# Performance work log

Hardware: AMD Instinct MI355X
Metric: run time of the kernel (lower is better)

Reference implementation:

```python
import jax, jax.numpy as jnp
import numpy as np

B, C, H, W = 4, 64, 256, 256
P, PRIOR, HID, HEADS, NPROMPT = 4, 64, 128, 4, 4
TOKEN = C * P * P  # 1024
RATIO = 0.25


def _patchify(x):
    b, c, h, w = x.shape
    gh, gw = h // P, w // P
    t = x.reshape(b, c, gh, P, gw, P).transpose(0, 2, 4, 1, 3, 5).reshape(b, gh * gw, c * P * P)
    return t, (b, c, gh, gw)


def _unpatchify(t, meta):
    b, c, gh, gw = meta
    return t.reshape(b, gh, gw, c, P, P).transpose(0, 3, 1, 4, 2, 5).reshape(b, c, gh * P, gw * P)


def _coords(gh, gw):
    ys = (jnp.arange(gh, dtype=jnp.float32) + 0.5) / gh
    xs = (jnp.arange(gw, dtype=jnp.float32) + 0.5) / gw
    yy, xx = jnp.meshgrid(ys, xs, indexing='ij')
    return jnp.stack([yy.ravel(), xx.ravel()], axis=-1)  # [N, 2]


def setup_inputs():
    key = jax.random.key(0)
    ks = iter(jax.random.split(key, 32))
    rn = lambda *s: jax.random.normal(next(ks), s, jnp.float32)
    w = lambda *s: rn(*s) * 0.02
    z = lambda *s: jnp.zeros(s, jnp.float32)
    return dict(
        vis_feat=rn(B, C, H, W),
        ir_feat=rn(B, C, H, W),
        prompt_bank=w(NPROMPT, PRIOR),
        Wr=w(2 * C, NPROMPT), br=z(NPROMPT),
        br_Wtok=w(2, 2 * TOKEN, HID), br_Wpri=w(2, PRIOR, HID), br_Wco=w(2, 2, HID),
        br_bs=z(2, HID), br_Wout=w(2, HID), br_bout=z(2),
        br_Wq=w(2, TOKEN, HID), br_Wk=w(2, TOKEN, HID), br_Wv=w(2, TOKEN, HID),
        br_Wo=w(2, HID, TOKEN), br_Wint=w(2, PRIOR, HID),
        br_Wbyp=w(2, 2 * TOKEN, TOKEN), br_bbyp=z(2, TOKEN),
        conv1_w=w(C, C, 3, 3), conv1_b=z(C),
        conv2_w=w(C, C, 3, 3), conv2_b=z(C),
        Wa1=w(PRIOR, 2 * C), ba1=z(2 * C),
        Wa2=w(2 * C, 2 * C), ba2=z(2 * C),
    )


def reference(vis_feat, ir_feat, prompt_bank, Wr, br, br_Wtok, br_Wpri, br_Wco, br_bs, br_Wout, br_bout, br_Wq, br_Wk, br_Wv, br_Wo, br_Wint, br_Wbyp, br_bbyp, conv1_w, conv1_b, conv2_w, conv2_b, Wa1, ba1, Wa2, ba2):
    # intent router: pooled features -> prompt mixture -> intent vector
    pooled = jnp.concatenate([vis_feat.mean((2, 3)), ir_feat.mean((2, 3))], -1)  # [B, 2C]
    prompt_weight = jax.nn.softmax(pooled @ Wr + br, -1)  # [B, NPROMPT]
    intent = prompt_weight @ prompt_bank  # [B, PRIOR]

    def split(x):
        F = jnp.fft.fft2(x)
        return jnp.abs(F), jnp.angle(F)

    vamp, vph = split(vis_feat)
    iamp, iph = split(ir_feat)

    def fuse(vm, im, i):
        vt, meta = _patchify(vm)
        it_, _ = _patchify(im)
        b, c, gh, gw = meta
        n = gh * gw
        coords = _coords(gh, gw)
        # token score net: tokens + intent + coord embedding -> scalar score per token
        h = (jnp.concatenate([vt, it_], -1) @ br_Wtok[i]
             + (intent @ br_Wpri[i])[:, None, :]
             + (coords @ br_Wco[i])[None] + br_bs[i])
        score = jax.nn.gelu(h) @ br_Wout[i] + br_bout[i]  # [B, N]
        k = max(1, int(n * RATIO))
        topk_val, topk_idx = jax.lax.top_k(score, k)
        gth = lambda t: jnp.take_along_axis(t, topk_idx[:, :, None], axis=1)
        vs, irs = gth(vt), gth(it_)  # [B, k, TOKEN]
        # selected-token cross attention (vis queries, ir keys/values), intent-modulated
        dh = HID // HEADS
        hd = lambda x, Wm: (x @ Wm).reshape(b, k, HEADS, dh)
        q, kk, vv = hd(vs, br_Wq[i]), hd(irs, br_Wk[i]), hd(irs, br_Wv[i])
        attn = jax.nn.softmax(jnp.einsum('bqhd,bkhd->bhqk', q, kk) / jnp.float32(np.sqrt(dh)), -1)
        o = jnp.einsum('bhqk,bkhd->bqhd', attn, vv).reshape(b, k, HID)
        o = o + (intent @ br_Wint[i])[:, None, :]
        fused_sel = vs + o @ br_Wo[i]  # [B, k, TOKEN]
        # lightweight bypass on all tokens (gated blend), then scatter selected back
        g = jax.nn.sigmoid(jnp.concatenate([vt, it_], -1) @ br_Wbyp[i] + br_bbyp[i])
        full = g * vt + (1.0 - g) * it_
        full = full.at[jnp.arange(b)[:, None], topk_idx].set(fused_sel)
        return _unpatchify(full, meta)

    famp = fuse(vamp, iamp, 0)
    fph = fuse(vph, iph, 1)
    fph = jnp.arctan2(jnp.sin(fph), jnp.cos(fph))  # phase wrap to (-pi, pi]
    spec = jax.lax.complex(famp * jnp.cos(fph), famp * jnp.sin(fph))
    spatial = jnp.fft.ifft2(spec).real

    conv = lambda x, wgt, bia: jax.lax.conv_general_dilated(
        x, wgt, (1, 1), 'SAME', dimension_numbers=('NCHW', 'OIHW', 'NCHW')) + bia[None, :, None, None]
    y = conv(jax.nn.relu(conv(spatial, conv1_w, conv1_b)), conv2_w, conv2_b)
    aff = jax.nn.gelu(intent @ Wa1 + ba1) @ Wa2 + ba2  # [B, 2C]
    gamma, beta = aff[:, :C], aff[:, C:]
    y = y * (1.0 + 0.1 * jnp.tanh(gamma))[:, :, None, None] + 0.1 * beta[:, :, None, None]
    return y + 0.5 * (vis_feat + ir_feat)
```

## Files before the change

kernel.cpp:

```cpp
#include <hip/hip_runtime.h>

typedef unsigned int uint;
typedef unsigned short ushort;
typedef unsigned long long u64;
typedef __attribute__((ext_vector_type(8))) short short8;
typedef __attribute__((ext_vector_type(4))) float f32x4;

__device__ __forceinline__ uint brev8(uint x){ return __brev(x) >> 24; }
__device__ __forceinline__ float geluf(float x){
  return 0.5f*x*(1.f + tanhf(0.7978845608028654f*(x + 0.044715f*x*x*x)));
}
__device__ __forceinline__ ushort f2bf(float f){
  unsigned u = __float_as_uint(f);
  unsigned r = u + 0x7FFFu + ((u >> 16) & 1u);
  return (ushort)(r >> 16);
}
__device__ __forceinline__ float bf2f(ushort u){
  return __uint_as_float((uint)u << 16);
}

__global__ __launch_bounds__(256) void kern_pool(const float* __restrict__ vis,
                                                 const float* __restrict__ irf,
                                                 float* __restrict__ pooled){
  __shared__ float red[256];
  int bc = blockIdx.x;
  int b = bc >> 7, cc = bc & 127;
  const float* src = (cc < 64) ? (vis + (size_t)(b*64+cc)*65536)
                               : (irf + (size_t)(b*64+(cc-64))*65536);
  float s = 0.f;
  for (int i = threadIdx.x; i < 65536; i += 256) s += src[i];
  red[threadIdx.x] = s;
  __syncthreads();
  for (int off = 128; off > 0; off >>= 1){
    if (threadIdx.x < off) red[threadIdx.x] += red[threadIdx.x + off];
    __syncthreads();
  }
  if (threadIdx.x == 0) pooled[bc] = red[0] * (1.f/65536.f);
}

__global__ __launch_bounds__(256) void kern_small(const float* __restrict__ pooled,
    const float* __restrict__ Wr, const float* __restrict__ br,
    const float* __restrict__ bank, const float* __restrict__ Wpri,
    const float* __restrict__ Wint, const float* __restrict__ Wa1,
    const float* __restrict__ ba1, const float* __restrict__ Wa2,
    const float* __restrict__ ba2,
    float* __restrict__ IP, float* __restrict__ IPint,
    float* __restrict__ modg, float* __restrict__ modb){
  __shared__ float logit_s[16];
  __shared__ float pw_s[16];
  __shared__ float intent_s[4][64];
  __shared__ float t1_s[4][128];
  int t = threadIdx.x;
  if (t < 16){
    int b = t >> 2, j = t & 3;
    float s = br[j];
    for (int k = 0; k < 128; ++k) s += pooled[b*128+k]*Wr[k*4+j];
    logit_s[t] = s;
  }
  __syncthreads();
  if (t < 4){
    int b = t;
    float m = logit_s[b*4];
    for (int j = 1; j < 4; ++j) m = fmaxf(m, logit_s[b*4+j]);
    float e[4], sum = 0.f;
    for (int j = 0; j < 4; ++j){ e[j] = expf(logit_s[b*4+j]-m); sum += e[j]; }
    for (int j = 0; j < 4; ++j) pw_s[b*4+j] = e[j]/sum;
  }
  __syncthreads();
  {
    int b = t >> 6, p = t & 63;
    float s = 0.f;
    for (int j = 0; j < 4; ++j) s += pw_s[b*4+j]*bank[j*64+p];
    intent_s[b][p] = s;
  }
  __syncthreads();
  for (int o = t; o < 1024; o += 256){
    int i = o >> 9, rem = o & 511, b = rem >> 7, n = rem & 127;
    float s1 = 0.f, s2 = 0.f;
    for (int p = 0; p < 64; ++p){
      float iv = intent_s[b][p];
      s1 += iv * Wpri[(i*64+p)*128 + n];
      s2 += iv * Wint[(i*64+p)*128 + n];
    }
    IP[o] = s1; IPint[o] = s2;
  }
  for (int o = t; o < 512; o += 256){
    int b = o >> 7, n = o & 127;
    float s = ba1[n];
    for (int p = 0; p < 64; ++p) s += intent_s[b][p]*Wa1[p*128+n];
    t1_s[b][n] = geluf(s);
  }
  __syncthreads();
  for (int o = t; o < 512; o += 256){
    int b = o >> 7, n = o & 127;
    float s = ba2[n];
    for (int p = 0; p < 128; ++p) s += t1_s[b][p]*Wa2[p*128+n];
    if (n < 64) modg[b*64+n] = 1.f + 0.1f*tanhf(s);
    else        modb[b*64+(n-64)] = 0.1f*s;
  }
}

__global__ __launch_bounds__(256) void kern_fft_rows_fwd(const float* __restrict__ x,
    float* __restrict__ sre, float* __restrict__ sim){
  __shared__ float re[2][256], im[2][256];
  __shared__ float twr[128], twi[128];
  int t = threadIdx.x;
  if (t < 128){
    float a = -6.2831853071795864f * (float)t * (1.f/256.f);
    sincosf(a, &twi[t], &twr[t]);
  }
  int r = t >> 7, jj = t & 127;
  size_t row = (size_t)blockIdx.x*2 + r;
  {
    const float* xp = x + row*256;
    re[r][jj] = xp[jj]; re[r][jj+128] = xp[jj+128];
    im[r][jj] = 0.f;    im[r][jj+128] = 0.f;
  }
  __syncthreads();
  for (int s = 0; s < 8; ++s){
    int half = 128 >> s;
    int j = jj & (half-1);
    int g = jj >> (7-s);
    int k = (g << (8-s)) + j;
    int m = j << s;
    float wc = twr[m], ws = twi[m];
    float are = re[r][k],      aim = im[r][k];
    float bre = re[r][k+half], bim = im[r][k+half];
    re[r][k] = are + bre; im[r][k] = aim + bim;
    float tr = are - bre, ti = aim - bim;
    re[r][k+half] = tr*wc - ti*ws;
    im[r][k+half] = tr*ws + ti*wc;
    __syncthreads();
  }
  {
    float* orp = sre + row*256; float* oip = sim + row*256;
    int w1 = jj, w2 = jj + 128;
    orp[w1] = re[r][brev8(w1)]; oip[w1] = im[r][brev8(w1)];
    orp[w2] = re[r][brev8(w2)]; oip[w2] = im[r][brev8(w2)];
  }
}

__global__ __launch_bounds__(256) void kern_ifft_rows_spec(const float* __restrict__ famp,
    const float* __restrict__ fph, float* __restrict__ sre, float* __restrict__ sim){
  __shared__ float re[4][256], im[4][256];
  __shared__ float twr[128], twi[128];
  int t = threadIdx.x;
  if (t < 128){
    float a = -6.2831853071795864f * (float)t * (1.f/256.f);
    sincosf(a, &twi[t], &twr[t]);
  }
  int R = blockIdx.x * 4;
  {
    int r = t >> 6, q = t & 63;
    int row = R + r;
    int bc = row >> 8, h = row & 255;
    int b = bc >> 6, c = bc & 63;
    size_t addr = ((size_t)(b*4096 + (h>>2)*64 + q))*1024 + c*16 + (h&3)*4;
    float4 a4 = *(const float4*)(famp + addr);
    float4 p4 = *(const float4*)(fph + addr);
    float sn, cs;
    sincosf(p4.x, &sn, &cs); re[r][4*q+0] = a4.x*cs; im[r][4*q+0] = a4.x*sn;
    sincosf(p4.y, &sn, &cs); re[r][4*q+1] = a4.y*cs; im[r][4*q+1] = a4.y*sn;
    sincosf(p4.z, &sn, &cs); re[r][4*q+2] = a4.z*cs; im[r][4*q+2] = a4.z*sn;
    sincosf(p4.w, &sn, &cs); re[r][4*q+3] = a4.w*cs; im[r][4*q+3] = a4.w*sn;
  }
  __syncthreads();
  for (int s = 0; s < 8; ++s){
    int half = 128 >> s;
    #pragma unroll
    for (int bi0 = 0; bi0 < 2; ++bi0){
      int bi = t + bi0*256;
      int r = bi >> 7, tj = bi & 127;
      int j = tj & (half-1);
      int g = tj >> (7-s);
      int k = (g << (8-s)) + j;
      int m = j << s;
      float wc = twr[m], ws = -twi[m];
      float are = re[r][k],      aim = im[r][k];
      float bre = re[r][k+half], bim = im[r][k+half];
      re[r][k] = are + bre; im[r][k] = aim + bim;
      float tr = are - bre, ti = aim - bim;
      re[r][k+half] = tr*wc - ti*ws;
      im[r][k+half] = tr*ws + ti*wc;
    }
    __syncthreads();
  }
  {
    int r = t >> 6, q = t & 63;
    size_t row = (size_t)R + r;
    float4 vr, vi;
    vr.x = re[r][brev8(4*q+0)]; vi.x = im[r][brev8(4*q+0)];
    vr.y = re[r][brev8(4*q+1)]; vi.y = im[r][brev8(4*q+1)];
    vr.z = re[r][brev8(4*q+2)]; vi.z = im[r][brev8(4*q+2)];
    vr.w = re[r][brev8(4*q+3)]; vi.w = im[r][brev8(4*q+3)];
    *(float4*)(sre + row*256 + 4*q) = vr;
    *(float4*)(sim + row*256 + 4*q) = vi;
  }
}

template<int DIR>
__global__ __launch_bounds__(256) void kern_fft_cols(const float* __restrict__ sre,
    const float* __restrict__ sim, void* __restrict__ out0, void* __restrict__ out1){
  __shared__ float reL[256*17];
  __shared__ float imL[256*17];
  __shared__ float twr[128], twi[128];
  int t = threadIdx.x;
  if (t < 128){
    float a = -6.2831853071795864f * (float)t * (1.f/256.f);
    sincosf(a, &twi[t], &twr[t]);
  }
  int img = blockIdx.x >> 4;
  int c0 = (blockIdx.x & 15) * 16;
  {
    const float* pr = sre + ((size_t)img*256 + t)*256 + c0;
    const float* pi = sim + ((size_t)img*256 + t)*256 + c0;
    #pragma unroll
    for (int p = 0; p < 4; ++p){
      float4 vr = *(const float4*)(pr + 4*p);
      float4 vi = *(const float4*)(pi + 4*p);
      int base = t*17 + 4*p;
      reL[base+0]=vr.x; reL[base+1]=vr.y; reL[base+2]=vr.z; reL[base+3]=vr.w;
      imL[base+0]=vi.x; imL[base+1]=vi.y; imL[base+2]=vi.z; imL[base+3]=vi.w;
    }
  }
  __syncthreads();
  int col = t & 15, tb = t >> 4;
  for (int s = 0; s < 8; ++s){
    int half = 128 >> s;
    #pragma unroll
    for (int it = 0; it < 8; ++it){
      int tj = tb + it*16;
      int j = tj & (half-1);
      int g = tj >> (7-s);
      int k = (g << (8-s)) + j;
      int m = j << s;
      float wc = twr[m];
      float ws = (DIR == 0) ? twi[m] : -twi[m];
      int i0 = k*17 + col, i1 = (k+half)*17 + col;
      float are = reL[i0], aim = imL[i0];
      float bre = reL[i1], bim = imL[i1];
      reL[i0] = are + bre; imL[i0] = aim + bim;
      float tr = are - bre, ti = aim - bim;
      reL[i1] = tr*wc - ti*ws;
      imL[i1] = tr*ws + ti*wc;
    }
    __syncthreads();
  }
  int b = img >> 6, c = img & 63;
  int h = t; int src = (int)brev8((uint)h);
  if (DIR == 0){
    ushort* oa = (ushort*)out0;
    ushort* op = (ushort*)out1;
    int gy = h >> 2, py = h & 3;
    #pragma unroll
    for (int p = 0; p < 4; ++p){
      int base = src*17 + 4*p;
      float a0, a1, a2, a3, p0, p1, p2, p3;
      float rr, ii;
      rr = reL[base+0]; ii = imL[base+0]; a0 = sqrtf(rr*rr+ii*ii); p0 = atan2f(ii, rr);
      rr = reL[base+1]; ii = imL[base+1]; a1 = sqrtf(rr*rr+ii*ii); p1 = atan2f(ii, rr);
      rr = reL[base+2]; ii = imL[base+2]; a2 = sqrtf(rr*rr+ii*ii); p2 = atan2f(ii, rr);
      rr = reL[base+3]; ii = imL[base+3]; a3 = sqrtf(rr*rr+ii*ii); p3 = atan2f(ii, rr);
      size_t addr = ((size_t)(b*4096 + gy*64 + (c0>>2) + p))*1024 + c*16 + py*4;
      uint2 av, pv;
      av.x = (uint)f2bf(a0) | ((uint)f2bf(a1) << 16);
      av.y = (uint)f2bf(a2) | ((uint)f2bf(a3) << 16);
      pv.x = (uint)f2bf(p0) | ((uint)f2bf(p1) << 16);
      pv.y = (uint)f2bf(p2) | ((uint)f2bf(p3) << 16);
      *(uint2*)(oa + addr) = av;
      *(uint2*)(op + addr) = pv;
    }
  } else {
    float* op = (float*)out0 + ((size_t)img*256 + h)*256 + c0;
    #pragma unroll
    for (int p = 0; p < 4; ++p){
      int base = src*17 + 4*p;
      float4 v;
      v.x = reL[base+0]*(1.f/65536.f);
      v.y = reL[base+1]*(1.f/65536.f);
      v.z = reL[base+2]*(1.f/65536.f);
      v.w = reL[base+3]*(1.f/65536.f);
      *(float4*)(op + 4*p) = v;
    }
  }
}

struct TRS {
  const float* src[10];
  ushort* dst[10];
  int K[10], N[10];
  int start[11];
};
__global__ __launch_bounds__(256) void kern_tr(TRS p){
  __shared__ float lds[32][33];
  int bid = blockIdx.x;
  int e = 0;
  while (bid >= p.start[e+1]) ++e;
  int tloc = bid - p.start[e];
  int tilesN = p.N[e] >> 5;
  int tn = tloc % tilesN, tk = tloc / tilesN;
  int k0 = tk << 5, n0 = tn << 5;
  const float* src = p.src[e];
  ushort* dst = p.dst[e];
  int K = p.K[e], N = p.N[e];
  int r = threadIdx.x >> 5, c = threadIdx.x & 31;
  #pragma unroll
  for (int i = 0; i < 4; ++i)
    lds[r + 8*i][c] = src[(size_t)(k0 + r + 8*i)*N + n0 + c];
  __syncthreads();
  #pragma unroll
  for (int i = 0; i < 4; ++i)
    dst[(size_t)(n0 + r + 8*i)*K + k0 + c] = f2bf(lds[c][r + 8*i]);
}

struct GP2 {
  const ushort* A0[6];
  const ushort* Bt[6];
  float* Cm[6];
  const int* idxp[6];
  int N, K;
};

__global__ __launch_bounds__(256) void kern_mgemm2(GP2 p){
  __shared__ __align__(16) ushort Asb[64*64];
  __shared__ __align__(16) ushort Bsb[128*64];
  __shared__ int idx_s[64];
  int z = blockIdx.z;
  const ushort* A0 = p.A0[z];
  const ushort* Bt = p.Bt[z];
  float* Cm = p.Cm[z];
  int tid = threadIdx.x;
  int m0 = blockIdx.x * 64;
  int n0 = blockIdx.y * 128;
  int lane = tid & 63, w = tid >> 6;
  int wr = w & 1, wc = w >> 1;
  int lr = lane & 15, ql = lane >> 4;

  if (tid < 64){
    int m = m0 + tid;
    idx_s[tid] = p.idxp[z][(m >> 10)*1024 + (m & 1023)];
  }
  __syncthreads();
  int gb = m0 >> 10;

  f32x4 acc[2][4];
  #pragma unroll
  for (int i = 0; i < 2; ++i)
    #pragma unroll
    for (int j = 0; j < 4; ++j) acc[i][j] = (f32x4){0.f,0.f,0.f,0.f};

  int kh = tid & 7;
  int rA = tid >> 3;
  for (int k0 = 0; k0 < p.K; k0 += 64){
    #pragma unroll
    for (int s = 0; s < 2; ++s){
      int m = rA + 32*s;
      const ushort* ap = A0 + ((size_t)(gb << 12) + idx_s[m])*(size_t)p.K + k0 + kh*8;
      short8 v = *(const short8*)ap;
      int byte = m*128 + ((kh*16) ^ ((m & 7)*16));
      *(short8*)((char*)Asb + byte) = v;
    }
    #pragma unroll
    for (int s = 0; s < 4; ++s){
      int n = rA + 32*s;
      short8 v = *(const short8*)(Bt + (size_t)(n0+n)*p.K + k0 + kh*8);
      int byte = n*128 + ((kh*16) ^ ((n & 7)*16));
      *(short8*)((char*)Bsb + byte) = v;
    }
    __syncthreads();
    short8 af[2][2], bf[4][2];
    #pragma unroll
    for (int fm = 0; fm < 2; ++fm){
      int row = wr*32 + fm*16 + lr;
      #pragma unroll
      for (int kq = 0; kq < 2; ++kq){
        int byte = row*128 + ((kq*64 + ql*16) ^ ((row & 7)*16));
        af[fm][kq] = *(const short8*)((const char*)Asb + byte);
      }
    }
    #pragma unroll
    for (int fn = 0; fn < 4; ++fn){
      int row = wc*64 + fn*16 + lr;
      #pragma unroll
      for (int kq = 0; kq < 2; ++kq){
        int byte = row*128 + ((kq*64 + ql*16) ^ ((row & 7)*16));
        bf[fn][kq] = *(const short8*)((const char*)Bsb + byte);
      }
    }
    #pragma unroll
    for (int kq = 0; kq < 2; ++kq)
      #pragma unroll
      for (int fm = 0; fm < 2; ++fm)
        #pragma unroll
        for (int fn = 0; fn < 4; ++fn)
          acc[fm][fn] = __builtin_amdgcn_mfma_f32_16x16x32_bf16(af[fm][kq], bf[fn][kq],
                                                                acc[fm][fn], 0, 0, 0);
    __syncthreads();
  }

  #pragma unroll
  for (int fm = 0; fm < 2; ++fm){
    #pragma unroll
    for (int fn = 0; fn < 4; ++fn){
      int n = n0 + wc*64 + fn*16 + lr;
      #pragma unroll
      for (int reg = 0; reg < 4; ++reg){
        int m = m0 + wr*32 + fm*16 + ql*4 + reg;
        Cm[(size_t)m*p.N + n] = acc[fm][fn][reg];
      }
    }
  }
}

struct HSP {
  const ushort* A0[2];
  const ushort* A1[2];
  const ushort* Bt[2];
  float* score;
  const float* ep0[2];
  const float* ep1[2];
  const float* ep2[2];
  const float* wout;
  const float* bout;
  int Mper;
};

__global__ __launch_bounds__(256) void kern_hscore(HSP p){
  __shared__ __align__(16) ushort Asb[128*64];
  __shared__ __align__(16) ushort Bsb[128*64];
  __shared__ float part[2][128];
  int z = blockIdx.z;
  const ushort* Bt = p.Bt[z];
  int tid = threadIdx.x;
  int m0 = blockIdx.x * 128;
  int lane = tid & 63, w = tid >> 6;
  int wr = w & 1, wc = w >> 1;
  int lr = lane & 15, ql = lane >> 4;

  f32x4 acc[4][4];
  #pragma unroll
  for (int i = 0; i < 4; ++i)
    #pragma unroll
    for (int j = 0; j < 4; ++j) acc[i][j] = (f32x4){0.f,0.f,0.f,0.f};

  int kh = tid & 7;
  int rA = tid >> 3;
  for (int k0 = 0; k0 < 2048; k0 += 64){
    const ushort* Asrc = (k0 < 1024) ? p.A0[z] : p.A1[z];
    int kk = (k0 & 1023) + kh*8;
    #pragma unroll
    for (int s = 0; s < 4; ++s){
      int m = rA + 32*s;
      short8 v = *(const short8*)(Asrc + (size_t)(m0+m)*1024 + kk);
      int byte = m*128 + ((kh*16) ^ ((m & 7)*16));
      *(short8*)((char*)Asb + byte) = v;
    }
    #pragma unroll
    for (int s = 0; s < 4; ++s){
      int n = rA + 32*s;
      short8 v = *(const short8*)(Bt + (size_t)n*2048 + k0 + kh*8);
      int byte = n*128 + ((kh*16) ^ ((n & 7)*16));
      *(short8*)((char*)Bsb + byte) = v;
    }
    __syncthreads();
    short8 af[4][2], bf[4][2];
    #pragma unroll
    for (int fm = 0; fm < 4; ++fm){
      int row = wr*64 + fm*16 + lr;
      #pragma unroll
      for (int kq = 0; kq < 2; ++kq){
        int byte = row*128 + ((kq*64 + ql*16) ^ ((row & 7)*16));
        af[fm][kq] = *(const short8*)((const char*)Asb + byte);
      }
    }
    #pragma unroll
    for (int fn = 0; fn < 4; ++fn){
      int row = wc*64 + fn*16 + lr;
      #pragma unroll
      for (int kq = 0; kq < 2; ++kq){
        int byte = row*128 + ((kq*64 + ql*16) ^ ((row & 7)*16));
        bf[fn][kq] = *(const short8*)((const char*)Bsb + byte);
      }
    }
    #pragma unroll
    for (int kq = 0; kq < 2; ++kq)
      #pragma unroll
      for (int fm = 0; fm < 4; ++fm)
        #pragma unroll
        for (int fn = 0; fn < 4; ++fn)
          acc[fm][fn] = __builtin_amdgcn_mfma_f32_16x16x32_bf16(af[fm][kq], bf[fn][kq],
                                                                acc[fm][fn], 0, 0, 0);
    __syncthreads();
  }

  float wv[4];
  #pragma unroll
  for (int fn = 0; fn < 4; ++fn) wv[fn] = p.wout[z*128 + wc*64 + fn*16 + lr];
  #pragma unroll
  for (int fm = 0; fm < 4; ++fm){
    #pragma unroll
    for (int reg = 0; reg < 4; ++reg){
      int m = m0 + wr*64 + fm*16 + ql*4 + reg;
      int bl = m >> 12, g = m & 4095;
      int gy = g >> 6, gx = g & 63;
      float cy = ((float)gy + 0.5f)*(1.f/64.f);
      float cx = ((float)gx + 0.5f)*(1.f/64.f);
      float ps = 0.f;
      #pragma unroll
      for (int fn = 0; fn < 4; ++fn){
        int n = wc*64 + fn*16 + lr;
        float o = acc[fm][fn][reg] + p.ep0[z][bl*128 + n] + cy*p.ep1[z][n]
                + cx*p.ep1[z][128 + n] + p.ep2[z][n];
        ps += geluf(o)*wv[fn];
      }
      #pragma unroll
      for (int off = 8; off > 0; off >>= 1) ps += __shfl_xor(ps, off);
      if (lr == 0) part[wc][wr*64 + fm*16 + ql*4 + reg] = ps;
    }
  }
  __syncthreads();
  if (tid < 128)
    p.score[(size_t)z*p.Mper + m0 + tid] = part[0][tid] + part[1][tid] + p.bout[z];
}

__global__ __launch_bounds__(1024) void kern_nsel(const int* __restrict__ idxb,
    int* __restrict__ nsel){
  __shared__ unsigned char mask[4096];
  __shared__ int cnt;
  int b = blockIdx.x, t = threadIdx.x;
  *(uint*)&mask[4*t] = 0;
  if (t == 0) cnt = 0;
  __syncthreads();
  mask[idxb[b*1024 + t]] = 1;
  __syncthreads();
  for (int i = t; i < 4096; i += 1024){
    if (!mask[i]){
      int pos = atomicAdd(&cnt, 1);
      nsel[(size_t)b*3072 + pos] = i;
    }
  }
}

struct BYP {
  const ushort* A0[2];
  const ushort* A1[2];
  const ushort* Bt[2];
  float* Cm[2];
  const int* nsel[2];
  const float* bias[2];
  const ushort* vt[2];
  const ushort* it[2];
};

__global__ __launch_bounds__(256) void kern_byp(BYP p){
  __shared__ __align__(16) ushort Asb[128*64];
  __shared__ __align__(16) ushort Bsb[128*64];
  __shared__ int idx_s[128];
  int z = blockIdx.z;
  const ushort* Bt = p.Bt[z];
  int tid = threadIdx.x;
  int gb  = blockIdx.x / 24;
  int m0l = (blockIdx.x % 24) * 128;
  int n0 = blockIdx.y * 128;
  int lane = tid & 63, w = tid >> 6;
  int wr = w & 1, wc = w >> 1;
  int lr = lane & 15, ql = lane >> 4;

  if (tid < 128)
    idx_s[tid] = p.nsel[z][(size_t)gb*3072 + m0l + tid];
  __syncthreads();

  f32x4 acc[4][4];
  #pragma unroll
  for (int i = 0; i < 4; ++i)
    #pragma unroll
    for (int j = 0; j < 4; ++j) acc[i][j] = (f32x4){0.f,0.f,0.f,0.f};

  int kh = tid & 7;
  int rA = tid >> 3;
  for (int k0 = 0; k0 < 2048; k0 += 64){
    const ushort* Asrc = (k0 < 1024) ? p.A0[z] : p.A1[z];
    int kk = (k0 & 1023) + kh*8;
    #pragma unroll
    for (int s = 0; s < 4; ++s){
      int m = rA + 32*s;
      size_t grow = (size_t)(gb << 12) + idx_s[m];
      short8 v = *(const short8*)(Asrc + grow*1024 + kk);
      int byte = m*128 + ((kh*16) ^ ((m & 7)*16));
      *(short8*)((char*)Asb + byte) = v;
    }
    #pragma unroll
    for (int s = 0; s < 4; ++s){
      int n = rA + 32*s;
      short8 v = *(const short8*)(Bt + (size_t)(n0+n)*2048 + k0 + kh*8);
      int byte = n*128 + ((kh*16) ^ ((n & 7)*16));
      *(short8*)((char*)Bsb + byte) = v;
    }
    __syncthreads();
    short8 af[4][2], bf[4][2];
    #pragma unroll
    for (int fm = 0; fm < 4; ++fm){
      int row = wr*64 + fm*16 + lr;
      #pragma unroll
      for (int kq = 0; kq < 2; ++kq){
        int byte = row*128 + ((kq*64 + ql*16) ^ ((row & 7)*16));
        af[fm][kq] = *(const short8*)((const char*)Asb + byte);
      }
    }
    #pragma unroll
    for (int fn = 0; fn < 4; ++fn){
      int row = wc*64 + fn*16 + lr;
      #pragma unroll
      for (int kq = 0; kq < 2; ++kq){
        int byte = row*128 + ((kq*64 + ql*16) ^ ((row & 7)*16));
        bf[fn][kq] = *(const short8*)((const char*)Bsb + byte);
      }
    }
    #pragma unroll
    for (int kq = 0; kq < 2; ++kq)
      #pragma unroll
      for (int fm = 0; fm < 4; ++fm)
        #pragma unroll
        for (int fn = 0; fn < 4; ++fn)
          acc[fm][fn] = __builtin_amdgcn_mfma_f32_16x16x32_bf16(af[fm][kq], bf[fn][kq],
                                                                acc[fm][fn], 0, 0, 0);
    __syncthreads();
  }

  float* Cm = p.Cm[z];
  const ushort* vtp = p.vt[z];
  const ushort* itp = p.it[z];
  #pragma unroll
  for (int fm = 0; fm < 4; ++fm){
    #pragma unroll
    for (int fn = 0; fn < 4; ++fn){
      int n = n0 + wc*64 + fn*16 + lr;
      float bia = p.bias[z][n];
      #pragma unroll
      for (int reg = 0; reg < 4; ++reg){
        int mloc = wr*64 + fm*16 + ql*4 + reg;
        size_t off = ((size_t)(gb << 12) + idx_s[mloc])*1024 + n;
        float vt = bf2f(vtp[off]);
        float it = bf2f(itp[off]);
        float gg = 1.f/(1.f + expf(-(acc[fm][fn][reg] + bia)));
        Cm[off] = gg*vt + (1.f-gg)*it;
      }
    }
  }
}

struct SCP {
  const float* A0[2];
  const float* Bm[2];
  float* Cm[2];
  const int* idxp[2];
  const ushort* vtb[2];
};

__global__ __launch_bounds__(256) void kern_scat(SCP p){
  __shared__ __align__(16) ushort Asb[64*40];
  __shared__ __align__(16) ushort Bsb[128*40];
  __shared__ int idx_s[64];
  int z = blockIdx.z;
  const float* A0 = p.A0[z];
  const float* Bm = p.Bm[z];
  float* Cm = p.Cm[z];
  int tid = threadIdx.x;
  int m0 = blockIdx.y * 64;
  int n0 = blockIdx.x * 128;
  int lane = tid & 63, w = tid >> 6;
  int wr = w & 1, wc = w >> 1;
  int lr = lane & 15, ql = lane >> 4;
  if (tid < 64){
    int m = m0 + tid;
    idx_s[tid] = p.idxp[z][(m >> 10)*1024 + (m & 1023)];
  }
  __syncthreads();
  int gb = m0 >> 10;

  f32x4 acc[2][4];
  #pragma unroll
  for (int i = 0; i < 2; ++i)
    #pragma unroll
    for (int j = 0; j < 4; ++j) acc[i][j] = (f32x4){0.f,0.f,0.f,0.f};

  for (int k0 = 0; k0 < 128; k0 += 32){
    {
      int m = tid & 63;
      int khh = (tid >> 6) * 8;
      const float* ap = A0 + (size_t)(m0+m)*128 + k0 + khh;
      float4 f0 = *(const float4*)ap;
      float4 f1 = *(const float4*)(ap + 4);
      short8 v;
      v[0]=(short)f2bf(f0.x); v[1]=(short)f2bf(f0.y);
      v[2]=(short)f2bf(f0.z); v[3]=(short)f2bf(f0.w);
      v[4]=(short)f2bf(f1.x); v[5]=(short)f2bf(f1.y);
      v[6]=(short)f2bf(f1.z); v[7]=(short)f2bf(f1.w);
      *(short8*)&Asb[m*40 + khh] = v;
    }
    #pragma unroll
    for (int e0 = 0; e0 < 512; e0 += 256){
      int e = e0 + tid;
      int n = e & 127;
      int khh = (e >> 7) * 8;
      const float* bp = Bm + (size_t)(k0+khh)*1024 + n0 + n;
      short8 v;
      #pragma unroll
      for (int j = 0; j < 8; ++j) v[j] = (short)f2bf(bp[(size_t)j*1024]);
      *(short8*)&Bsb[n*40 + khh] = v;
    }
    __syncthreads();
    short8 af[2], bf[4];
    #pragma unroll
    for (int fr = 0; fr < 2; ++fr)
      af[fr] = *(const short8*)&Asb[(wr*32 + fr*16 + lr)*40 + ql*8];
    #pragma unroll
    for (int fc = 0; fc < 4; ++fc)
      bf[fc] = *(const short8*)&Bsb[(wc*64 + fc*16 + lr)*40 + ql*8];
    #pragma unroll
    for (int fr = 0; fr < 2; ++fr)
      #pragma unroll
      for (int fc = 0; fc < 4; ++fc)
        acc[fr][fc] = __builtin_amdgcn_mfma_f32_16x16x32_bf16(af[fr], bf[fc],
                                                              acc[fr][fc], 0, 0, 0);
    __syncthreads();
  }

  #pragma unroll
  for (int fr = 0; fr < 2; ++fr){
    #pragma unroll
    for (int fc = 0; fc < 4; ++fc){
      int n = n0 + wc*64 + fc*16 + lr;
      #pragma unroll
      for (int reg = 0; reg < 4; ++reg){
        int mloc = wr*32 + fr*16 + ql*4 + reg;
        int gt = idx_s[mloc];
        size_t off = ((size_t)(gb << 12) + gt)*1024 + n;
        Cm[off] = acc[fr][fc][reg] + bf2f(p.vtb[z][off]);
      }
    }
  }
}

__global__ __launch_bounds__(1024) void kern_topk(const float* __restrict__ score,
    int* __restrict__ idx_out){
  __shared__ u64 keys[4096];
  int b = blockIdx.x, t = threadIdx.x;
  for (int i = t; i < 4096; i += 1024){
    float s = score[b*4096 + i];
    uint u = __float_as_uint(s);
    uint msk = (u & 0x80000000u) ? ~u : (u | 0x80000000u);
    keys[i] = ((u64)msk << 32) | (uint)(4095 - i);
  }
  __syncthreads();
  for (int k = 2; k <= 4096; k <<= 1){
    for (int j = k >> 1; j > 0; j >>= 1){
      for (int i = t; i < 4096; i += 1024){
        int l = i ^ j;
        if (l > i){
          u64 a = keys[i], c = keys[l];
          bool descB = ((i & k) == 0);
          bool sw = descB ? (a < c) : (a > c);
          if (sw){ keys[i] = c; keys[l] = a; }
        }
      }
      __syncthreads();
    }
  }
  idx_out[b*1024 + t] = 4095 - (int)(keys[t] & 0xFFFFFFFFu);
}

__global__ __launch_bounds__(128) void kern_attn_part(const float* __restrict__ qb,
    const float* __restrict__ kb, const float* __restrict__ vb,
    float* __restrict__ paoa, float* __restrict__ pml){
  __shared__ float Ks[64][32];
  __shared__ float Vs[64][32];
  int t = threadIdx.x;
  int hh = blockIdx.y;
  int zc = blockIdx.z;
  int zf = zc >> 2, c = zc & 3;
  size_t boff = (size_t)zf*131072;
  int jq = blockIdx.x*128 + t;
  float qv[32];
  {
    const float4* qp = (const float4*)(qb + boff + (size_t)jq*128 + hh*32);
    #pragma unroll
    for (int d = 0; d < 8; ++d) ((float4*)qv)[d] = qp[d];
  }
  float mrun = -3.0e38f, lrun = 0.f;
  float oa[32];
  #pragma unroll
  for (int d = 0; d < 32; ++d) oa[d] = 0.f;
  for (int kt = 0; kt < 4; ++kt){
    int k0 = c*256 + kt*64;
    #pragma unroll
    for (int rep = 0; rep < 4; ++rep){
      int f = t + rep*128;
      int r = f >> 3, q4 = f & 7;
      size_t base = boff + (size_t)(k0 + r)*128 + hh*32 + 4*q4;
      *(float4*)&Ks[r][4*q4] = *(const float4*)(kb + base);
      *(float4*)&Vs[r][4*q4] = *(const float4*)(vb + base);
    }
    __syncthreads();
    #pragma unroll
    for (int st = 0; st < 4; ++st){
      float s[16];
      #pragma unroll
      for (int j = 0; j < 16; ++j){
        float v = 0.f;
        #pragma unroll
        for (int d = 0; d < 32; ++d) v += qv[d]*Ks[st*16+j][d];
        s[j] = v * 0.17677669529663687f;
      }
      float mt = s[0];
      #pragma unroll
      for (int j = 1; j < 16; ++j) mt = fmaxf(mt, s[j]);
      float mnew = fmaxf(mrun, mt);
      float alpha = expf(mrun - mnew);
      lrun *= alpha;
      #pragma unroll
      for (int d = 0; d < 32; ++d) oa[d] *= alpha;
      #pragma unroll
      for (int j = 0; j < 16; ++j){
        float pe = expf(s[j] - mnew);
        lrun += pe;
        #pragma unroll
        for (int d = 0; d < 32; ++d) oa[d] += pe*Vs[st*16+j][d];
      }
      mrun = mnew;
    }
    __syncthreads();
  }
  size_t rec = (((size_t)zf*4 + hh)*4 + c)*1024 + jq;
  float* pp = paoa + rec*32;
  #pragma unroll
  for (int d = 0; d < 8; ++d) ((float4*)pp)[d] = ((float4*)oa)[d];
  pml[rec*2]   = mrun;
  pml[rec*2+1] = lrun;
}

__global__ __launch_bounds__(256) void kern_attn_comb(const float* __restrict__ paoa,
    const float* __restrict__ pml, float* __restrict__ ob,
    const float* __restrict__ ipint, int PB, int b0){
  int t = threadIdx.x;
  int hh = blockIdx.y, zf = blockIdx.z;
  int jq = blockIdx.x*256 + t;
  size_t rbase = (((size_t)zf*4 + hh)*4)*1024 + jq;
  float mc[4], lc[4];
  #pragma unroll
  for (int c = 0; c < 4; ++c){
    mc[c] = pml[(rbase + c*1024)*2];
    lc[c] = pml[(rbase + c*1024)*2 + 1];
  }
  float M = fmaxf(fmaxf(mc[0], mc[1]), fmaxf(mc[2], mc[3]));
  float wgt[4], L = 0.f;
  #pragma unroll
  for (int c = 0; c < 4; ++c){ wgt[c] = expf(mc[c] - M); L += lc[c]*wgt[c]; }
  float inv = 1.f/L;
  int br = (zf >= PB) ? 1 : 0;
  int bb = zf - br*PB;
  const float* ip = ipint + br*512 + (b0+bb)*128 + hh*32;
  float* op = ob + (size_t)zf*131072 + (size_t)jq*128 + hh*32;
  #pragma unroll
  for (int d = 0; d < 32; ++d){
    float o = 0.f;
    #pragma unroll
    for (int c = 0; c < 4; ++c) o += paoa[(rbase + c*1024)*32 + d]*wgt[c];
    op[d] = o*inv + ip[d];
  }
}

__global__ __launch_bounds__(256) void kern_wt(const float* __restrict__ w1,
    const float* __restrict__ w2, ushort* __restrict__ wt){
  int blk = blockIdx.x;
  const float* src = (blk < 9) ? w1 : w2;
  int tap = blk - (blk < 9 ? 0 : 9);
  ushort* dst = wt + (blk < 9 ? 0 : 36864) + tap*4096;
  for (int e = threadIdx.x; e < 4096; e += 256){
    dst[e] = f2bf(src[(size_t)e*9 + tap]);
  }
}

template<int MODE>
__global__ __launch_bounds__(256) void kern_cmfma(const float* __restrict__ in,
    const ushort* __restrict__ wt, const float* __restrict__ bias,
    float* __restrict__ out,
    const float* __restrict__ modg, const float* __restrict__ modb,
    const float* __restrict__ vis, const float* __restrict__ irf){
  __shared__ __align__(16) ushort ins[64][268];
  int t = threadIdx.x;
  int y = blockIdx.x, b = blockIdx.y;
  int lane = t & 63, w = t >> 6;
  int wc = w & 1, wx = w >> 1;
  int lr = lane & 15, ql = lane >> 4;

  f32x4 acc[2][8];
  #pragma unroll
  for (int f = 0; f < 2; ++f)
    #pragma unroll
    for (int xf = 0; xf < 8; ++xf) acc[f][xf] = (f32x4){0.f,0.f,0.f,0.f};

  for (int dy = 0; dy < 3; ++dy){
    int yy = y + dy - 1;
    if (yy < 0 || yy > 255) continue;
    const float* src = in + ((size_t)(b*64)*256 + yy)*256;
    #pragma unroll
    for (int s = 0; s < 16; ++s){
      int e = t + s*256;
      int ci = e >> 6, q = e & 63;
      float4 f4 = *(const float4*)(src + (size_t)ci*65536 + 4*q);
      uint lo = (uint)f2bf(f4.x) | ((uint)f2bf(f4.y) << 16);
      uint hi = (uint)f2bf(f4.z) | ((uint)f2bf(f4.w) << 16);
      *(uint2*)&ins[ci][4*q + 4] = make_uint2(lo, hi);
    }
    if (t < 128){
      int r = t & 63;
      ins[r][(t >> 6) ? 260 : 3] = 0;
    }
    __syncthreads();
    short8 wf[2][3][2];
    #pragma unroll
    for (int kk = 0; kk < 2; ++kk)
      #pragma unroll
      for (int dx = 0; dx < 3; ++dx)
        #pragma unroll
        for (int f = 0; f < 2; ++f)
          wf[kk][dx][f] = *(const short8*)(wt +
            (size_t)((dy*3 + dx)*64 + 32*wc + 16*f + lr)*64 + kk*32 + ql*8);
    #pragma unroll
    for (int kk = 0; kk < 2; ++kk){
      const ushort* bp = &ins[kk*32 + ql*8][0];
      #pragma unroll
      for (int dx = 0; dx < 3; ++dx){
        int xb = 128*wx + lr + dx + 3;
        #pragma unroll
        for (int xf = 0; xf < 8; ++xf){
          int xi = xb + 16*xf;
          short8 bf;
          #pragma unroll
          for (int e = 0; e < 8; ++e) bf[e] = (short)bp[e*268 + xi];
          acc[0][xf] = __builtin_amdgcn_mfma_f32_16x16x32_bf16(wf[kk][dx][0], bf,
                                                               acc[0][xf], 0, 0, 0);
          acc[1][xf] = __builtin_amdgcn_mfma_f32_16x16x32_bf16(wf[kk][dx][1], bf,
                                                               acc[1][xf], 0, 0, 0);
        }
      }
    }
    __syncthreads();
  }

  #pragma unroll
  for (int f = 0; f < 2; ++f){
    #pragma unroll
    for (int xf = 0; xf < 8; ++xf){
      int x = 128*wx + 16*xf + lr;
      #pragma unroll
      for (int reg = 0; reg < 4; ++reg){
        int co = 32*wc + 16*f + ql*4 + reg;
        float v = acc[f][xf][reg] + bias[co];
        size_t oi = ((size_t)(b*64 + co)*256 + y)*256 + x;
        if (MODE == 1){
          out[oi] = fmaxf(v, 0.f);
        } else {
          out[oi] = v*modg[b*64+co] + modb[b*64+co] + 0.5f*(vis[oi] + irf[oi]);
        }
      }
    }
  }
}

extern "C" void kernel_launch(void* const* d_in, const int* in_sizes, int n_in,
                              void* d_out, int out_size, void* d_ws, size_t ws_size,
                              hipStream_t stream){
  (void)in_sizes; (void)n_in; (void)out_size;
  const float* vis  = (const float*)d_in[0];
  const float* irf  = (const float*)d_in[1];
  const float* bank = (const float*)d_in[2];
  const float* Wr   = (const float*)d_in[3];
  const float* br   = (const float*)d_in[4];
  const float* Wtok = (const float*)d_in[5];
  const float* Wpri = (const float*)d_in[6];
  const float* Wco  = (const float*)d_in[7];
  const float* bs   = (const float*)d_in[8];
  const float* Wout = (const float*)d_in[9];
  const float* bout = (const float*)d_in[10];
  const float* Wq   = (const float*)d_in[11];
  const float* Wk   = (const float*)d_in[12];
  const float* Wv   = (const float*)d_in[13];
  const float* Wo   = (const float*)d_in[14];
  const float* Wint = (const float*)d_in[15];
  const float* Wbyp = (const float*)d_in[16];
  const float* bbyp = (const float*)d_in[17];
  const float* c1w  = (const float*)d_in[18];
  const float* c1b  = (const float*)d_in[19];
  const float* c2w  = (const float*)d_in[20];
  const float* c2b  = (const float*)d_in[21];
  const float* Wa1  = (const float*)d_in[22];
  const float* ba1  = (const float*)d_in[23];
  const float* Wa2  = (const float*)d_in[24];
  const float* ba2  = (const float*)d_in[25];

  auto needB = [](int PB)->size_t{
    return ((size_t)PB*14755840 + 2792448) * 4;
  };
  const int PB = (ws_size >= needB(4)) ? 4 : (ws_size >= needB(2)) ? 2 : 1;

  float* ws = (float*)d_ws;
  const size_t PLF = (size_t)PB*4194304;
  float* PH4 = ws;
  ushort* ABV = (ushort*)(ws + PLF);
  ushort* PBV = ABV + PLF;
  ushort* ABI = PBV + PLF;
  ushort* PBI = ABI + PLF;
  float* S0 = ws + PLF;
  float* S1 = S0 + PLF;
  float* sm = ws + 3*PLF;
  float* hbuf  = sm; sm += (size_t)2*PB*524288;
  float* qbuf  = sm; sm += (size_t)2*PB*131072;
  float* kbuf  = sm; sm += (size_t)2*PB*131072;
  float* vbuf  = sm; sm += (size_t)2*PB*131072;
  float* obuf  = sm; sm += (size_t)2*PB*131072;
  float* score = sm; sm += (size_t)2*PB*4096;
  int*   idxb  = (int*)sm; sm += (size_t)2*PB*1024;
  float* pml   = sm; sm += (size_t)PB*65536;
  ushort* BTtok = (ushort*)sm;
  ushort* BTbyp = BTtok + 524288;
  ushort* BTq   = BTbyp + 4194304;
  ushort* BTk   = BTq + 262144;
  ushort* BTv   = BTk + 262144;
  sm += 2752512;
  float* pooled= sm; sm += 512;
  float* IP    = sm; sm += 1024;
  float* IPint = sm; sm += 1024;
  float* modg  = sm; sm += 256;
  float* modb  = sm; sm += 256;
  ushort* wtb = (ushort*)sm; sm += 36864;
  int*   nselb = (int*)hbuf;
  float* paoa  = hbuf;

  kern_pool <<<512, 256, 0, stream>>>(vis, irf, pooled);
  kern_small<<<1, 256, 0, stream>>>(pooled, Wr, br, bank, Wpri, Wint,
                                    Wa1, ba1, Wa2, ba2, IP, IPint, modg, modb);
  kern_wt   <<<18, 256, 0, stream>>>(c1w, c2w, wtb);
  {
    TRS tr{};
    const float* srcs[10] = {Wtok, Wtok+262144, Wbyp, Wbyp+2097152,
                             Wq, Wq+131072, Wk, Wk+131072, Wv, Wv+131072};
    ushort* dsts[10] = {BTtok, BTtok+262144, BTbyp, BTbyp+2097152,
                        BTq, BTq+131072, BTk, BTk+131072, BTv, BTv+131072};
    int Ks[10] = {2048,2048,2048,2048,1024,1024,1024,1024,1024,1024};
    int Ns[10] = {128,128,1024,1024,128,128,128,128,128,128};
    int tiles[10] = {256,256,2048,2048,128,128,128,128,128,128};
    int acc0 = 0;
    for (int i = 0; i < 10; ++i){
      tr.src[i] = srcs[i]; tr.dst[i] = dsts[i];
      tr.K[i] = Ks[i]; tr.N[i] = Ns[i];
      tr.start[i] = acc0; acc0 += tiles[i];
    }
    tr.start[10] = acc0;
    kern_tr<<<acc0, 256, 0, stream>>>(tr);
  }

  for (int b0 = 0; b0 < 4; b0 += PB){
    const float* vis_b = vis + (size_t)b0*4194304;
    const float* ir_b  = irf + (size_t)b0*4194304;
    float* OUT = (float*)d_out + (size_t)b0*4194304;

    kern_fft_rows_fwd<<<PB*8192, 256, 0, stream>>>(vis_b, OUT, PH4);
    kern_fft_cols<0> <<<PB*1024, 256, 0, stream>>>(OUT, PH4, ABV, PBV);
    kern_fft_rows_fwd<<<PB*8192, 256, 0, stream>>>(ir_b, OUT, PH4);
    kern_fft_cols<0> <<<PB*1024, 256, 0, stream>>>(OUT, PH4, ABI, PBI);

    {
      HSP p{};
      p.A0[0]=ABV; p.A1[0]=ABI; p.A0[1]=PBV; p.A1[1]=PBI;
      for (int z = 0; z < 2; ++z){
        p.Bt[z] = BTtok + (size_t)z*262144;
        p.ep0[z] = IP + z*512 + b0*128;
        p.ep1[z] = Wco + z*256;
        p.ep2[z] = bs + z*128;
      }
      p.score = score; p.wout = Wout; p.bout = bout;
      p.Mper = PB*4096;
      kern_hscore<<<dim3(PB*32, 1, 2), 256, 0, stream>>>(p);
    }
    kern_topk<<<2*PB, 1024, 0, stream>>>(score, idxb);
    kern_nsel<<<2*PB, 1024, 0, stream>>>(idxb, nselb);
    {
      BYP p{};
      p.A0[0]=ABV; p.A1[0]=ABI; p.A0[1]=PBV; p.A1[1]=PBI;
      p.vt[0]=ABV; p.it[0]=ABI; p.vt[1]=PBV; p.it[1]=PBI;
      p.Cm[0]=OUT; p.Cm[1]=PH4;
      for (int z = 0; z < 2; ++z){
        p.Bt[z] = BTbyp + (size_t)z*2097152;
        p.bias[z] = bbyp + z*1024;
        p.nsel[z] = nselb + (size_t)z*PB*3072;
      }
      kern_byp<<<dim3(PB*24, 8, 2), 256, 0, stream>>>(p);
    }
    {
      GP2 p{};
      const ushort* Aplanes[6] = {ABV, ABI, ABI, PBV, PBI, PBI};
      const ushort* Bmats[6] = {BTq, BTk, BTv, BTq+131072, BTk+131072, BTv+131072};
      float* Cms[6] = {qbuf, kbuf, vbuf,
                       qbuf+(size_t)PB*131072, kbuf+(size_t)PB*131072,
                       vbuf+(size_t)PB*131072};
      for (int z = 0; z < 6; ++z){
        p.A0[z] = Aplanes[z]; p.Bt[z] = Bmats[z]; p.Cm[z] = Cms[z];
        p.idxp[z] = idxb + (z < 3 ? 0 : PB*1024);
      }
      p.N = 128; p.K = 1024;
      kern_mgemm2<<<dim3(PB*16, 1, 6), 256, 0, stream>>>(p);
    }
    kern_attn_part<<<dim3(8, 4, 2*PB*4), 128, 0, stream>>>(qbuf, kbuf, vbuf,
                                                           paoa, pml);
    kern_attn_comb<<<dim3(4, 4, 2*PB), 256, 0, stream>>>(paoa, pml, obuf,
                                                         IPint, PB, b0);
    {
      SCP p{};
      p.A0[0]=obuf; p.A0[1]=obuf+(size_t)PB*131072;
      p.Bm[0]=Wo; p.Bm[1]=Wo+131072;
      p.Cm[0]=OUT; p.Cm[1]=PH4;
      p.vtb[0]=ABV; p.vtb[1]=PBV;
      p.idxp[0]=idxb; p.idxp[1]=idxb+PB*1024;
      kern_scat<<<dim3(8, PB*16, 2), 256, 0, stream>>>(p);
    }

    kern_ifft_rows_spec<<<PB*4096, 256, 0, stream>>>(OUT, PH4, S0, S1);
    kern_fft_cols<1>   <<<PB*1024, 256, 0, stream>>>(S0, S1, OUT, nullptr);
  }

  kern_cmfma<1><<<dim3(256, 4), 256, 0, stream>>>((float*)d_out, wtb, c1b, ws,
                                                  nullptr, nullptr, nullptr, nullptr);
  kern_cmfma<2><<<dim3(256, 4), 256, 0, stream>>>(ws, wtb + 36864, c2b, (float*)d_out,
                                                  modg, modb, vis, irf);
}
```

Baseline: 1.365 ms.

## Pack vis and IR into one complex FFT and fold nsel into topk

Two real inputs are now packed as real and imaginary parts of a single complex 2D FFT. Hermitian symmetry is used in the column pass to separate the two spectra before computing amplitude and phase. This halves the forward FFT row and column work and launches. The non-selected index list is written straight from the sorted keys in topk, which removes the separate nsel kernel. The cost is scalar bf16 scatter stores instead of vectorized ones, plus extra conjugate-pair loads and some precision risk from the packing.

After: 1.291 ms. 1.06x faster.

```diff
diff --git a/kernel.cpp b/kernel.cpp
--- a/kernel.cpp
+++ b/kernel.cpp
@@ -100,8 +100,8 @@
   }
 }
 
-__global__ __launch_bounds__(256) void kern_fft_rows_fwd(const float* __restrict__ x,
-    float* __restrict__ sre, float* __restrict__ sim){
+__global__ __launch_bounds__(256) void kern_fft_rows_pack(const float* __restrict__ xv,
+    const float* __restrict__ xi, float* __restrict__ sre, float* __restrict__ sim){
   __shared__ float re[2][256], im[2][256];
   __shared__ float twr[128], twi[128];
   int t = threadIdx.x;
@@ -112,9 +112,10 @@
   int r = t >> 7, jj = t & 127;
   size_t row = (size_t)blockIdx.x*2 + r;
   {
-    const float* xp = x + row*256;
-    re[r][jj] = xp[jj]; re[r][jj+128] = xp[jj+128];
-    im[r][jj] = 0.f;    im[r][jj+128] = 0.f;
+    const float* vp = xv + row*256;
+    const float* ip = xi + row*256;
+    re[r][jj] = vp[jj]; re[r][jj+128] = vp[jj+128];
+    im[r][jj] = ip[jj]; im[r][jj+128] = ip[jj+128];
   }
   __syncthreads();
   for (int s = 0; s < 8; ++s){
@@ -137,6 +138,103 @@
     int w1 = jj, w2 = jj + 128;
     orp[w1] = re[r][brev8(w1)]; oip[w1] = im[r][brev8(w1)];
     orp[w2] = re[r][brev8(w2)]; oip[w2] = im[r][brev8(w2)];
+  }
+}
+
+__global__ __launch_bounds__(256) void kern_fft_cols_pack(const float* __restrict__ sre,
+    const float* __restrict__ sim, ushort* __restrict__ AV, ushort* __restrict__ PV,
+    ushort* __restrict__ AI, ushort* __restrict__ PI){
+  __shared__ float reL[256*17];
+  __shared__ float imL[256*17];
+  __shared__ float twr[128], twi[128];
+  int t = threadIdx.x;
+  if (t < 128){
+    float a = -6.2831853071795864f * (float)t * (1.f/256.f);
+    sincosf(a, &twi[t], &twr[t]);
+  }
+  int img = blockIdx.x >> 4;
+  int j = blockIdx.x & 15;
+  {
+    const float* pr = sre + ((size_t)img*256 + t)*256;
+    const float* pi = sim + ((size_t)img*256 + t)*256;
+    int base = t*17;
+    float4 a0 = *(const float4*)(pr + 8*j);
+    float4 a1 = *(const float4*)(pr + 8*j + 4);
+    float4 c0 = *(const float4*)(pi + 8*j);
+    float4 c1 = *(const float4*)(pi + 8*j + 4);
+    reL[base+0]=a0.x; reL[base+1]=a0.y; reL[base+2]=a0.z; reL[base+3]=a0.w;
+    reL[base+4]=a1.x; reL[base+5]=a1.y; reL[base+6]=a1.z; reL[base+7]=a1.w;
+    imL[base+0]=c0.x; imL[base+1]=c0.y; imL[base+2]=c0.z; imL[base+3]=c0.w;
+    imL[base+4]=c1.x; imL[base+5]=c1.y; imL[base+6]=c1.z; imL[base+7]=c1.w;
+    if (j == 0){
+      reL[base+8] = pr[128]; imL[base+8] = pi[128];
+      float4 b0 = *(const float4*)(pr + 248);
+      float4 b1 = *(const float4*)(pr + 252);
+      float4 d0 = *(const float4*)(pi + 248);
+      float4 d1 = *(const float4*)(pi + 252);
+      reL[base+9]=b0.y;  reL[base+10]=b0.z; reL[base+11]=b0.w;
+      reL[base+12]=b1.x; reL[base+13]=b1.y; reL[base+14]=b1.z; reL[base+15]=b1.w;
+      imL[base+9]=d0.y;  imL[base+10]=d0.z; imL[base+11]=d0.w;
+      imL[base+12]=d1.x; imL[base+13]=d1.y; imL[base+14]=d1.z; imL[base+15]=d1.w;
+    } else {
+      float4 b0 = *(const float4*)(pr + 248 - 8*j);
+      float4 b1 = *(const float4*)(pr + 252 - 8*j);
+      float4 d0 = *(const float4*)(pi + 248 - 8*j);
+      float4 d1 = *(const float4*)(pi + 252 - 8*j);
+      reL[base+8]=b0.y;  reL[base+9]=b0.z;  reL[base+10]=b0.w;
+      reL[base+11]=b1.x; reL[base+12]=b1.y; reL[base+13]=b1.z; reL[base+14]=b1.w;
+      reL[base+15]=pr[256 - 8*j];
+      imL[base+8]=d0.y;  imL[base+9]=d0.z;  imL[base+10]=d0.w;
+      imL[base+11]=d1.x; imL[base+12]=d1.y; imL[base+13]=d1.z; imL[base+14]=d1.w;
+      imL[base+15]=pi[256 - 8*j];
+    }
+  }
+  __syncthreads();
+  int col = t & 15, tb = t >> 4;
+  for (int s = 0; s < 8; ++s){
+    int half = 128 >> s;
+    #pragma unroll
+    for (int it = 0; it < 8; ++it){
+      int tj = tb + it*16;
+      int jl = tj & (half-1);
+      int g = tj >> (7-s);
+      int k = (g << (8-s)) + jl;
+      int m = jl << s;
+      float wc = twr[m], ws = twi[m];
+      int i0 = k*17 + col, i1 = (k+half)*17 + col;
+      float are = reL[i0], aim = imL[i0];
+      float bre = reL[i1], bim = imL[i1];
+      reL[i0] = are + bre; imL[i0] = aim + bim;
+      float tr = are - bre, ti = aim - bim;
+      reL[i1] = tr*wc - ti*ws;
+      imL[i1] = tr*ws + ti*wc;
+    }
+    __syncthreads();
+  }
+  int b = img >> 6, cimg = img & 63;
+  int u = t;
+  int su  = (int)brev8((uint)u) * 17;
+  int smu = (int)brev8((uint)((256 - u) & 255)) * 17;
+  #pragma unroll
+  for (int c = 0; c < 16; ++c){
+    int v, mc;
+    if (j == 0){
+      v  = (c < 8) ? c : ((c == 8) ? 128 : 240 + c);
+      mc = (c == 0) ? 0 : ((c == 8) ? 8 : 16 - c);
+    } else {
+      v  = (c < 8) ? (8*j + c) : (241 - 8*j + c);
+      mc = 15 - c;
+    }
+    float re1 = reL[su + c],  im1 = imL[su + c];
+    float re2 = reL[smu + mc], im2 = imL[smu + mc];
+    float vr = 0.5f*(re1 + re2), vi = 0.5f*(im1 - im2);
+    float jr = 0.5f*(im1 + im2), ji = 0.5f*(re2 - re1);
+    float aV = sqrtf(vr*vr + vi*vi), pVh = atan2f(vi, vr);
+    float aI = sqrtf(jr*jr + ji*ji), pIh = atan2f(ji, jr);
+    size_t addr = ((size_t)(b*4096 + (u>>2)*64 + (v>>2)))*1024
+                + cimg*16 + (u&3)*4 + (v&3);
+    AV[addr] = f2bf(aV); PV[addr] = f2bf(pVh);
+    AI[addr] = f2bf(aI); PI[addr] = f2bf(pIh);
   }
 }
 
@@ -198,9 +296,8 @@
   }
 }
 
-template<int DIR>
-__global__ __launch_bounds__(256) void kern_fft_cols(const float* __restrict__ sre,
-    const float* __restrict__ sim, void* __restrict__ out0, void* __restrict__ out1){
+__global__ __launch_bounds__(256) void kern_fft_cols_inv(const float* __restrict__ sre,
+    const float* __restrict__ sim, float* __restrict__ out0){
   __shared__ float reL[256*17];
   __shared__ float imL[256*17];
   __shared__ float twr[128], twi[128];
@@ -235,7 +332,7 @@
       int k = (g << (8-s)) + j;
       int m = j << s;
       float wc = twr[m];
-      float ws = (DIR == 0) ? twi[m] : -twi[m];
+      float ws = -twi[m];
       int i0 = k*17 + col, i1 = (k+half)*17 + col;
       float are = reL[i0], aim = imL[i0];
       float bre = reL[i1], bim = imL[i1];
@@ -246,42 +343,17 @@
     }
     __syncthreads();
   }
-  int b = img >> 6, c = img & 63;
   int h = t; int src = (int)brev8((uint)h);
-  if (DIR == 0){
-    ushort* oa = (ushort*)out0;
-    ushort* op = (ushort*)out1;
-    int gy = h >> 2, py = h & 3;
-    #pragma unroll
-    for (int p = 0; p < 4; ++p){
-      int base = src*17 + 4*p;
-      float a0, a1, a2, a3, p0, p1, p2, p3;
-      float rr, ii;
-      rr = reL[base+0]; ii = imL[base+0]; a0 = sqrtf(rr*rr+ii*ii); p0 = atan2f(ii, rr);
-      rr = reL[base+1]; ii = imL[base+1]; a1 = sqrtf(rr*rr+ii*ii); p1 = atan2f(ii, rr);
-      rr = reL[base+2]; ii = imL[base+2]; a2 = sqrtf(rr*rr+ii*ii); p2 = atan2f(ii, rr);
-      rr = reL[base+3]; ii = imL[base+3]; a3 = sqrtf(rr*rr+ii*ii); p3 = atan2f(ii, rr);
-      size_t addr = ((size_t)(b*4096 + gy*64 + (c0>>2) + p))*1024 + c*16 + py*4;
-      uint2 av, pv;
-      av.x = (uint)f2bf(a0) | ((uint)f2bf(a1) << 16);
-      av.y = (uint)f2bf(a2) | ((uint)f2bf(a3) << 16);
-      pv.x = (uint)f2bf(p0) | ((uint)f2bf(p1) << 16);
-      pv.y = (uint)f2bf(p2) | ((uint)f2bf(p3) << 16);
-      *(uint2*)(oa + addr) = av;
-      *(uint2*)(op + addr) = pv;
-    }
-  } else {
-    float* op = (float*)out0 + ((size_t)img*256 + h)*256 + c0;
-    #pragma unroll
-    for (int p = 0; p < 4; ++p){
-      int base = src*17 + 4*p;
-      float4 v;
-      v.x = reL[base+0]*(1.f/65536.f);
-      v.y = reL[base+1]*(1.f/65536.f);
-      v.z = reL[base+2]*(1.f/65536.f);
-      v.w = reL[base+3]*(1.f/65536.f);
-      *(float4*)(op + 4*p) = v;
-    }
+  float* op = out0 + ((size_t)img*256 + h)*256 + c0;
+  #pragma unroll
+  for (int p = 0; p < 4; ++p){
+    int base = src*17 + 4*p;
+    float4 v;
+    v.x = reL[base+0]*(1.f/65536.f);
+    v.y = reL[base+1]*(1.f/65536.f);
+    v.z = reL[base+2]*(1.f/65536.f);
+    v.w = reL[base+3]*(1.f/65536.f);
+    *(float4*)(op + 4*p) = v;
   }
 }
 
@@ -523,24 +595,6 @@
     p.score[(size_t)z*p.Mper + m0 + tid] = part[0][tid] + part[1][tid] + p.bout[z];
 }
 
-__global__ __launch_bounds__(1024) void kern_nsel(const int* __restrict__ idxb,
-    int* __restrict__ nsel){
-  __shared__ unsigned char mask[4096];
-  __shared__ int cnt;
-  int b = blockIdx.x, t = threadIdx.x;
-  *(uint*)&mask[4*t] = 0;
-  if (t == 0) cnt = 0;
-  __syncthreads();
-  mask[idxb[b*1024 + t]] = 1;
-  __syncthreads();
-  for (int i = t; i < 4096; i += 1024){
-    if (!mask[i]){
-      int pos = atomicAdd(&cnt, 1);
-      nsel[(size_t)b*3072 + pos] = i;
-    }
-  }
-}
-
 struct BYP {
   const ushort* A0[2];
   const ushort* A1[2];
@@ -743,7 +797,7 @@
 }
 
 __global__ __launch_bounds__(1024) void kern_topk(const float* __restrict__ score,
-    int* __restrict__ idx_out){
+    int* __restrict__ idx_out, int* __restrict__ nsel_out){
   __shared__ u64 keys[4096];
   int b = blockIdx.x, t = threadIdx.x;
   for (int i = t; i < 4096; i += 1024){
@@ -768,6 +822,8 @@
     }
   }
   idx_out[b*1024 + t] = 4095 - (int)(keys[t] & 0xFFFFFFFFu);
+  for (int i = t; i < 3072; i += 1024)
+    nsel_out[(size_t)b*3072 + i] = 4095 - (int)(keys[1024 + i] & 0xFFFFFFFFu);
 }
 
 __global__ __launch_bounds__(128) void kern_attn_part(const float* __restrict__ qb,
@@ -1066,10 +1122,8 @@
     const float* ir_b  = irf + (size_t)b0*4194304;
     float* OUT = (float*)d_out + (size_t)b0*4194304;
 
-    kern_fft_rows_fwd<<<PB*8192, 256, 0, stream>>>(vis_b, OUT, PH4);
-    kern_fft_cols<0> <<<PB*1024, 256, 0, stream>>>(OUT, PH4, ABV, PBV);
-    kern_fft_rows_fwd<<<PB*8192, 256, 0, stream>>>(ir_b, OUT, PH4);
-    kern_fft_cols<0> <<<PB*1024, 256, 0, stream>>>(OUT, PH4, ABI, PBI);
+    kern_fft_rows_pack<<<PB*8192, 256, 0, stream>>>(vis_b, ir_b, OUT, PH4);
+    kern_fft_cols_pack<<<PB*1024, 256, 0, stream>>>(OUT, PH4, ABV, PBV, ABI, PBI);
 
     {
       HSP p{};
@@ -1084,8 +1138,7 @@
       p.Mper = PB*4096;
       kern_hscore<<<dim3(PB*32, 1, 2), 256, 0, stream>>>(p);
     }
-    kern_topk<<<2*PB, 1024, 0, stream>>>(score, idxb);
-    kern_nsel<<<2*PB, 1024, 0, stream>>>(idxb, nselb);
+    kern_topk<<<2*PB, 1024, 0, stream>>>(score, idxb, nselb);
     {
       BYP p{};
       p.A0[0]=ABV; p.A1[0]=ABI; p.A0[1]=PBV; p.A1[1]=PBI;
@@ -1127,7 +1180,7 @@
     }
 
     kern_ifft_rows_spec<<<PB*4096, 256, 0, stream>>>(OUT, PH4, S0, S1);
-    kern_fft_cols<1>   <<<PB*1024, 256, 0, stream>>>(S0, S1, OUT, nullptr);
+    kern_fft_cols_inv  <<<PB*1024, 256, 0, stream>>>(S0, S1, OUT);
   }
 
   kern_cmfma<1><<<dim3(256, 4), 256, 0, stream>>>((float*)d_out, wtb, c1b, ws,
```
